# Optimization experiments

Hardware: AMD Instinct MI355X
Metric: run time of the kernel (lower is better)

Reference implementation:

```python
import jax, jax.numpy as jnp
import numpy as np

TOP_K = 2


def setup_inputs() -> dict:
    key = jax.random.key(0)
    k1, k2, k3, k4 = jax.random.split(key, 4)
    B, S, D, F, E = 4, 512, 512, 2048, 16
    hidden_states = jax.random.normal(k1, (B, S, D), dtype=jnp.float32)
    gate_weight = jax.random.normal(k2, (E, D), dtype=jnp.float32) * 0.02
    w1 = jax.random.normal(k3, (E, F, D), dtype=jnp.float32) * 0.02
    w2 = jax.random.normal(k4, (E, D, F), dtype=jnp.float32) * 0.02
    return {"hidden_states": hidden_states, "gate_weight": gate_weight, "w1": w1, "w2": w2}


def reference(hidden_states, gate_weight, w1, w2):
    B, S, D = hidden_states.shape
    E = gate_weight.shape[0]
    x = hidden_states.reshape(-1, D)  # [T, D]

    # fused_top_k_routing: logits = x @ Wg^T, top-k, softmax over the k values
    gate_logits = x @ gate_weight.T  # [T, E]
    top_vals, top_idx = jax.lax.top_k(gate_logits, TOP_K)  # [T, k]
    routing_w = jax.nn.softmax(top_vals, axis=-1)  # [T, k]

    # _prepare_expert_inputs: token t goes to expert e iff e in its top-k
    mask = jnp.any(top_idx[:, :, None] == jnp.arange(E)[None, None, :], axis=1)  # [T, E] bool

    # Expert FFN on routed tokens, computed densely over (token, expert) pairs then masked.
    # h[t,e,f] = silu(x_t @ W1_e^T)
    h = jax.nn.silu(jnp.einsum('td,efd->tef', x, w1))  # [T, E, F]
    counts = jnp.sum(mask, axis=0)  # [E]
    h_sum = jnp.einsum('tef,te->ef', h, mask.astype(h.dtype))  # [E, F]
    h_mean = h_sum / jnp.maximum(counts, 1)[:, None].astype(h.dtype)

    # fused_expert_scatter_gather uses expert_outputs[e].mean(dim=0);
    # mean(W2 @ act) = W2 @ mean(act) since W2 is linear.
    y_mean = jnp.einsum('ef,edf->ed', h_mean, w2)  # [E, D]
    y_mean = jnp.where((counts > 0)[:, None], y_mean, 0.0)

    # per-token combine: sum_k w_k * mean_output[expert_k]
    out = jnp.einsum('tk,tkd->td', routing_w, y_mean[top_idx])  # [T, D]
    return out.reshape(B, S, D)
```

## Files before the change

kernel.cpp:

```cpp
#include <hip/hip_runtime.h>

#define NTOK   2048
#define DIM    512
#define FDIM   2048
#define NEXP   16
#define CAP    768
#define BT2    128
#define NTB    (CAP / BT2)

typedef __bf16 bf16x8 __attribute__((ext_vector_type(8)));
typedef __bf16 bf16x4 __attribute__((ext_vector_type(4)));
typedef float  floatx4 __attribute__((ext_vector_type(4)));

#define WS_COUNTS    0
#define WS_ZEROPAGE  1024
#define WS_TOPIDX    4096
#define WS_ROUTW     20480
#define WS_HMEAN     36864
#define WS_YMEAN     167936
#define WS_XG        200704
#define WS_ZERO_BYTES 167936

__global__ __launch_bounds__(256) void k1_route_gather(
    const float* __restrict__ x, const float* __restrict__ gw,
    int* __restrict__ counts, int* __restrict__ top_idx,
    float* __restrict__ routw, __bf16* __restrict__ Xg)
{
    __shared__ float xt[16 * DIM];
    __shared__ float lg[16][17];
    __shared__ int   gdst[16][2];
    const int tid = threadIdx.x;
    const int t0  = blockIdx.x * 16;

    {
        const float4* src = (const float4*)(x + (size_t)t0 * DIM);
        float4* dst = (float4*)xt;
        #pragma unroll
        for (int i = 0; i < 8; ++i) dst[i * 256 + tid] = src[i * 256 + tid];
    }
    __syncthreads();

    {
        const int tl = tid >> 4, e = tid & 15;
        const float4* xr = (const float4*)(xt + tl * DIM);
        const float4* gr = (const float4*)(gw + e * DIM);
        float acc = 0.f;
        #pragma unroll 8
        for (int j = 0; j < DIM / 4; ++j) {
            float4 a = xr[j], b = gr[j];
            acc += a.x * b.x + a.y * b.y + a.z * b.z + a.w * b.w;
        }
        lg[tl][e] = acc;
    }
    __syncthreads();

    if (tid < 16) {
        const int tl = tid;
        float v0 = -1e30f, v1 = -1e30f; int i0 = 0, i1 = 0;
        #pragma unroll
        for (int e = 0; e < NEXP; ++e) {
            float v = lg[tl][e];
            if (v > v0)      { v1 = v0; i1 = i0; v0 = v; i0 = e; }
            else if (v > v1) { v1 = v;  i1 = e; }
        }
        float e1 = __expf(v1 - v0);
        float w0 = 1.f / (1.f + e1);
        float w1 = 1.f - w0;
        const int t = t0 + tl;
        top_idx[t * 2]     = i0; top_idx[t * 2 + 1] = i1;
        routw[t * 2]       = w0; routw[t * 2 + 1]   = w1;
        int p0 = atomicAdd(counts + i0, 1);
        int p1 = atomicAdd(counts + i1, 1);
        gdst[tl][0] = (p0 < CAP) ? (i0 * CAP + p0) : -1;
        gdst[tl][1] = (p1 < CAP) ? (i1 * CAP + p1) : -1;
    }
    __syncthreads();

    #pragma unroll
    for (int it = 0; it < 16; ++it) {
        int s   = it * 256 + tid;
        int job = s >> 7, el = s & 127;
        int tl  = job >> 1, k = job & 1;
        int dst = gdst[tl][k];
        if (dst >= 0) {
            float4 v = ((const float4*)(xt + tl * DIM))[el];
            bf16x4 o = { (__bf16)v.x, (__bf16)v.y, (__bf16)v.z, (__bf16)v.w };
            *(bf16x4*)(Xg + (size_t)dst * DIM + el * 4) = o;
        }
    }
}

__global__ __launch_bounds__(256) void k2_expert_ffn(
    const float* __restrict__ w1, const __bf16* __restrict__ Xg,
    const int* __restrict__ counts, const __bf16* __restrict__ zp,
    float* __restrict__ hmean)
{
    __shared__ __align__(16) __bf16 w1s[8 * 65 * 8];
    __shared__ __align__(16) __bf16 xs[8 * 129 * 8];
    __shared__ float hred[64][2];

    const int tid = threadIdx.x;
    const int bid = blockIdx.x;
    const int tb  = bid >> 9;
    const int rem = bid & 511;
    const int e   = rem & 15;
    const int f0  = (rem >> 4) * 64;
    const int cnt = min(counts[e], CAP);
    if (tb * BT2 >= cnt) return;
    const float inv = 1.f / (float)cnt;

    const int wv   = tid >> 6;
    const int lane = tid & 63;
    const int q    = lane >> 4;
    const int l15  = lane & 15;
    const int fsub = (wv & 1) * 32;
    const int tsub = (wv >> 1) * 64;

    floatx4 acc[2][4];
    #pragma unroll
    for (int a = 0; a < 2; ++a)
        #pragma unroll
        for (int b = 0; b < 4; ++b) acc[a][b] = (floatx4)0.f;

    for (int c = 0; c < 8; ++c) {
        const int d0 = c * 64;
        __syncthreads();
        #pragma unroll
        for (int it = 0; it < 2; ++it) {
            int s = it * 256 + tid;
            int f = s >> 3, g = s & 7;
            const float* src = w1 + ((size_t)(e * FDIM + f0 + f)) * DIM + d0 + g * 8;
            float4 a = ((const float4*)src)[0];
            float4 b = ((const float4*)src)[1];
            bf16x8 v;
            v[0] = (__bf16)a.x; v[1] = (__bf16)a.y; v[2] = (__bf16)a.z; v[3] = (__bf16)a.w;
            v[4] = (__bf16)b.x; v[5] = (__bf16)b.y; v[6] = (__bf16)b.z; v[7] = (__bf16)b.w;
            *(bf16x8*)(w1s + ((size_t)g * 65 + f) * 8) = v;
        }
        {
            const int kg = tid & 7;
            const int r0 = tid >> 3;
            #pragma unroll
            for (int it = 0; it < 4; ++it) {
                int t = it * 32 + r0;
                int r = tb * BT2 + t;
                const __bf16* src = (r < cnt)
                    ? (Xg + ((size_t)(e * CAP + r)) * DIM + d0 + kg * 8)
                    : zp;
                uint4 d = *(const uint4*)src;
                *(uint4*)(xs + ((size_t)kg * 129 + t) * 8) = d;
            }
        }
        __syncthreads();
        #pragma unroll
        for (int ks = 0; ks < 2; ++ks) {
            const int kg = ks * 4 + q;
            bf16x8 af0 = *(const bf16x8*)(w1s + (kg * 65 + fsub + l15) * 8);
            bf16x8 af1 = *(const bf16x8*)(w1s + (kg * 65 + fsub + 16 + l15) * 8);
            #pragma unroll
            for (int tt = 0; tt < 4; ++tt) {
                bf16x8 bfr = *(const bf16x8*)(xs + (kg * 129 + tsub + tt * 16 + l15) * 8);
                acc[0][tt] = __builtin_amdgcn_mfma_f32_16x16x32_bf16(af0, bfr, acc[0][tt], 0, 0, 0);
                acc[1][tt] = __builtin_amdgcn_mfma_f32_16x16x32_bf16(af1, bfr, acc[1][tt], 0, 0, 0);
            }
        }
    }

    float hs[8];
    #pragma unroll
    for (int i = 0; i < 8; ++i) hs[i] = 0.f;
    #pragma unroll
    for (int fa = 0; fa < 2; ++fa)
        #pragma unroll
        for (int tt = 0; tt < 4; ++tt)
            #pragma unroll
            for (int r = 0; r < 4; ++r) {
                float v = acc[fa][tt][r];
                hs[fa * 4 + r] += v / (1.f + __expf(-v));
            }

    #pragma unroll
    for (int i = 0; i < 8; ++i) {
        float v = hs[i];
        v += __shfl_xor(v, 1);
        v += __shfl_xor(v, 2);
        v += __shfl_xor(v, 4);
        v += __shfl_xor(v, 8);
        hs[i] = v;
    }
    if (l15 == 0) {
        #pragma unroll
        for (int fa = 0; fa < 2; ++fa)
            #pragma unroll
            for (int r = 0; r < 4; ++r) {
                int row = fsub + fa * 16 + q * 4 + r;
                hred[row][wv >> 1] = hs[fa * 4 + r];
            }
    }
    __syncthreads();
    if (tid < 64)
        atomicAdd(hmean + (size_t)e * FDIM + f0 + tid,
                  (hred[tid][0] + hred[tid][1]) * inv);
}

__global__ __launch_bounds__(256) void k3_ymean(
    const float* __restrict__ w2, const float* __restrict__ hmean,
    const int* __restrict__ counts, float* __restrict__ ymean)
{
    __shared__ float hl[FDIM];
    const int tid = threadIdx.x;
    const int bid = blockIdx.x;
    const int e   = bid >> 7;
    const int d0  = (bid & 127) * 4;

    {
        const float4* hg = (const float4*)(hmean + (size_t)e * FDIM);
        float4* hl4 = (float4*)hl;
        hl4[tid]       = hg[tid];
        hl4[256 + tid] = hg[256 + tid];
    }
    __syncthreads();

    const int wv = tid >> 6, lane = tid & 63;
    const int d = d0 + wv;
    const float4* wr  = (const float4*)(w2 + ((size_t)e * DIM + d) * FDIM);
    const float4* hl4 = (const float4*)hl;
    float acc = 0.f;
    #pragma unroll
    for (int i = 0; i < 8; ++i) {
        float4 a = wr[i * 64 + lane];
        float4 h = hl4[i * 64 + lane];
        acc += a.x * h.x + a.y * h.y + a.z * h.z + a.w * h.w;
    }
    #pragma unroll
    for (int m = 1; m < 64; m <<= 1) acc += __shfl_xor(acc, m);
    if (lane == 0)
        ymean[e * DIM + d] = (counts[e] > 0) ? acc : 0.f;
}

__global__ __launch_bounds__(256) void k4_combine(
    const int* __restrict__ top_idx, const float* __restrict__ routw,
    const float* __restrict__ ymean, float* __restrict__ out)
{
    const int idx = blockIdx.x * 256 + threadIdx.x;
    const int t = idx >> 7;
    const int c = idx & 127;
    const int i0 = top_idx[t * 2], i1 = top_idx[t * 2 + 1];
    const float w0 = routw[t * 2], w1 = routw[t * 2 + 1];
    float4 a = ((const float4*)(ymean + (size_t)i0 * DIM))[c];
    float4 b = ((const float4*)(ymean + (size_t)i1 * DIM))[c];
    float4 o;
    o.x = w0 * a.x + w1 * b.x;
    o.y = w0 * a.y + w1 * b.y;
    o.z = w0 * a.z + w1 * b.z;
    o.w = w0 * a.w + w1 * b.w;
    ((float4*)out)[idx] = o;
}

extern "C" void kernel_launch(void* const* d_in, const int* in_sizes, int n_in,
                              void* d_out, int out_size, void* d_ws, size_t ws_size,
                              hipStream_t stream)
{
    (void)in_sizes; (void)n_in; (void)out_size; (void)ws_size;
    const float* x  = (const float*)d_in[0];
    const float* gw = (const float*)d_in[1];
    const float* w1 = (const float*)d_in[2];
    const float* w2 = (const float*)d_in[3];
    float* out = (float*)d_out;

    char* ws = (char*)d_ws;
    int*    counts  = (int*)   (ws + WS_COUNTS);
    const __bf16* zp = (const __bf16*)(ws + WS_ZEROPAGE);
    int*    top_idx = (int*)   (ws + WS_TOPIDX);
    float*  routw   = (float*) (ws + WS_ROUTW);
    float*  hmean   = (float*) (ws + WS_HMEAN);
    float*  ymean   = (float*) (ws + WS_YMEAN);
    __bf16* Xg      = (__bf16*)(ws + WS_XG);

    hipMemsetAsync(d_ws, 0, WS_ZERO_BYTES, stream);

    k1_route_gather<<<dim3(NTOK / 16), dim3(256), 0, stream>>>(x, gw, counts, top_idx, routw, Xg);
    k2_expert_ffn  <<<dim3(NTB * 32 * NEXP), dim3(256), 0, stream>>>(w1, Xg, counts, zp, hmean);
    k3_ymean       <<<dim3(NEXP * 128), dim3(256), 0, stream>>>(w2, hmean, counts, ymean);
    k4_combine     <<<dim3(NTOK * DIM / 4 / 256), dim3(256), 0, stream>>>(top_idx, routw, ymean, out);
}
```

Measured before the change: 212.9 us.

## Restructure expert FFN: resident W1 slice, loop token chunks with async double-buffered loads

Each block now owns a 32-wide F slice of one expert and keeps the full W1 slice (all of D) in shared memory, converted to bf16 once. It then loops over every token chunk for that expert, staging activations with async global-to-LDS loads into a double buffer. Before, W1 was reloaded for every token tile. Because one block now covers all tokens for its slice, the atomicAdd becomes a plain store and the memset shrinks to just the counts region. The cost is fewer blocks (1024) whose work grows with the expert's token count, which risks load imbalance across experts and lower occupancy from the larger LDS footprint.

```diff
diff --git a/kernel.cpp b/kernel.cpp
--- a/kernel.cpp
+++ b/kernel.cpp
@@ -5,8 +5,8 @@
 #define FDIM   2048
 #define NEXP   16
 #define CAP    768
-#define BT2    128
-#define NTB    (CAP / BT2)
+#define FT     32
+#define TC     128
 
 typedef __bf16 bf16x8 __attribute__((ext_vector_type(8)));
 typedef __bf16 bf16x4 __attribute__((ext_vector_type(4)));
@@ -19,7 +19,13 @@
 #define WS_HMEAN     36864
 #define WS_YMEAN     167936
 #define WS_XG        200704
-#define WS_ZERO_BYTES 167936
+#define WS_ZERO_BYTES 2048
+
+__device__ __forceinline__ void async_lds16(const void* g, void* l) {
+    __builtin_amdgcn_global_load_lds(
+        (__attribute__((address_space(1))) void*)(void*)g,
+        (__attribute__((address_space(3))) void*)l, 16, 0, 0);
+}
 
 __global__ __launch_bounds__(256) void k1_route_gather(
     const float* __restrict__ x, const float* __restrict__ gw,
@@ -95,112 +101,118 @@
     const int* __restrict__ counts, const __bf16* __restrict__ zp,
     float* __restrict__ hmean)
 {
-    __shared__ __align__(16) __bf16 w1s[8 * 65 * 8];
-    __shared__ __align__(16) __bf16 xs[8 * 129 * 8];
-    __shared__ float hred[64][2];
+    __shared__ __align__(16) __bf16 w1s[64 * 33 * 8];
+    __shared__ __align__(16) __bf16 xs[2][8 * 128 * 8];
+    __shared__ float hred[FT][4];
 
     const int tid = threadIdx.x;
     const int bid = blockIdx.x;
-    const int tb  = bid >> 9;
-    const int rem = bid & 511;
-    const int e   = rem & 15;
-    const int f0  = (rem >> 4) * 64;
+    const int e   = ((bid & 7) << 1) | (bid >> 9);
+    const int f0  = ((bid >> 3) & 63) * FT;
     const int cnt = min(counts[e], CAP);
-    if (tb * BT2 >= cnt) return;
-    const float inv = 1.f / (float)cnt;
+    const float inv = 1.f / (float)max(cnt, 1);
 
     const int wv   = tid >> 6;
     const int lane = tid & 63;
     const int q    = lane >> 4;
     const int l15  = lane & 15;
-    const int fsub = (wv & 1) * 32;
-    const int tsub = (wv >> 1) * 64;
-
-    floatx4 acc[2][4];
+    const int tsub = wv * 32;
+
+    const int nchunk = (cnt + TC - 1) / TC;
+    const int total  = nchunk * 8;
+
+    auto STAGE = [&](int b, int tc, int c) {
+        __bf16* dst0 = xs[b];
+        #pragma unroll
+        for (int it = 0; it < 4; ++it) {
+            int base = it * 256 + wv * 64;
+            int slot = base + lane;
+            int kg = slot >> 7, t = slot & 127;
+            int r  = tc * TC + t;
+            const __bf16* src = (r < cnt)
+                ? (Xg + ((size_t)(e * CAP + r)) * DIM + c * 64 + kg * 8)
+                : zp;
+            async_lds16(src, dst0 + (size_t)base * 8);
+        }
+    };
+
+    if (total > 0) STAGE(0, 0, 0);
+
+    #pragma unroll
+    for (int it = 0; it < 8; ++it) {
+        int s = it * 256 + tid;
+        int kg = s & 63, f = s >> 6;
+        const float* src = w1 + ((size_t)(e * FDIM + f0 + f)) * DIM + kg * 8;
+        float4 a = ((const float4*)src)[0];
+        float4 b = ((const float4*)src)[1];
+        bf16x8 v;
+        v[0] = (__bf16)a.x; v[1] = (__bf16)a.y; v[2] = (__bf16)a.z; v[3] = (__bf16)a.w;
+        v[4] = (__bf16)b.x; v[5] = (__bf16)b.y; v[6] = (__bf16)b.z; v[7] = (__bf16)b.w;
+        *(bf16x8*)(w1s + ((size_t)kg * 33 + f) * 8) = v;
+    }
+    __syncthreads();
+
+    floatx4 acc[2][2];
     #pragma unroll
     for (int a = 0; a < 2; ++a)
         #pragma unroll
-        for (int b = 0; b < 4; ++b) acc[a][b] = (floatx4)0.f;
-
-    for (int c = 0; c < 8; ++c) {
-        const int d0 = c * 64;
+        for (int b = 0; b < 2; ++b) acc[a][b] = (floatx4)0.f;
+    float rs[2][4] = {{0.f, 0.f, 0.f, 0.f}, {0.f, 0.f, 0.f, 0.f}};
+
+    for (int g = 0; g < total; ++g) {
+        const int cur = g & 1;
+        const int c   = g & 7;
+        if (g + 1 < total) STAGE(cur ^ 1, (g + 1) >> 3, (g + 1) & 7);
+
+        const __bf16* xb = xs[cur];
+        #pragma unroll
+        for (int ks = 0; ks < 2; ++ks) {
+            int kga = c * 8 + ks * 4 + q;
+            int kl  = ks * 4 + q;
+            bf16x8 a0 = *(const bf16x8*)(w1s + ((size_t)kga * 33 + l15) * 8);
+            bf16x8 a1 = *(const bf16x8*)(w1s + ((size_t)kga * 33 + 16 + l15) * 8);
+            bf16x8 b0 = *(const bf16x8*)(xb + ((size_t)kl * 128 + tsub + l15) * 8);
+            bf16x8 b1 = *(const bf16x8*)(xb + ((size_t)kl * 128 + tsub + 16 + l15) * 8);
+            acc[0][0] = __builtin_amdgcn_mfma_f32_16x16x32_bf16(a0, b0, acc[0][0], 0, 0, 0);
+            acc[0][1] = __builtin_amdgcn_mfma_f32_16x16x32_bf16(a0, b1, acc[0][1], 0, 0, 0);
+            acc[1][0] = __builtin_amdgcn_mfma_f32_16x16x32_bf16(a1, b0, acc[1][0], 0, 0, 0);
+            acc[1][1] = __builtin_amdgcn_mfma_f32_16x16x32_bf16(a1, b1, acc[1][1], 0, 0, 0);
+        }
+        if (c == 7) {
+            #pragma unroll
+            for (int fa = 0; fa < 2; ++fa)
+                #pragma unroll
+                for (int r = 0; r < 4; ++r) {
+                    float v0 = acc[fa][0][r], v1 = acc[fa][1][r];
+                    rs[fa][r] += v0 / (1.f + __expf(-v0)) + v1 / (1.f + __expf(-v1));
+                    acc[fa][0][r] = 0.f; acc[fa][1][r] = 0.f;
+                }
+        }
         __syncthreads();
-        #pragma unroll
-        for (int it = 0; it < 2; ++it) {
-            int s = it * 256 + tid;
-            int f = s >> 3, g = s & 7;
-            const float* src = w1 + ((size_t)(e * FDIM + f0 + f)) * DIM + d0 + g * 8;
-            float4 a = ((const float4*)src)[0];
-            float4 b = ((const float4*)src)[1];
-            bf16x8 v;
-            v[0] = (__bf16)a.x; v[1] = (__bf16)a.y; v[2] = (__bf16)a.z; v[3] = (__bf16)a.w;
-            v[4] = (__bf16)b.x; v[5] = (__bf16)b.y; v[6] = (__bf16)b.z; v[7] = (__bf16)b.w;
-            *(bf16x8*)(w1s + ((size_t)g * 65 + f) * 8) = v;
-        }
-        {
-            const int kg = tid & 7;
-            const int r0 = tid >> 3;
-            #pragma unroll
-            for (int it = 0; it < 4; ++it) {
-                int t = it * 32 + r0;
-                int r = tb * BT2 + t;
-                const __bf16* src = (r < cnt)
-                    ? (Xg + ((size_t)(e * CAP + r)) * DIM + d0 + kg * 8)
-                    : zp;
-                uint4 d = *(const uint4*)src;
-                *(uint4*)(xs + ((size_t)kg * 129 + t) * 8) = d;
-            }
-        }
-        __syncthreads();
-        #pragma unroll
-        for (int ks = 0; ks < 2; ++ks) {
-            const int kg = ks * 4 + q;
-            bf16x8 af0 = *(const bf16x8*)(w1s + (kg * 65 + fsub + l15) * 8);
-            bf16x8 af1 = *(const bf16x8*)(w1s + (kg * 65 + fsub + 16 + l15) * 8);
-            #pragma unroll
-            for (int tt = 0; tt < 4; ++tt) {
-                bf16x8 bfr = *(const bf16x8*)(xs + (kg * 129 + tsub + tt * 16 + l15) * 8);
-                acc[0][tt] = __builtin_amdgcn_mfma_f32_16x16x32_bf16(af0, bfr, acc[0][tt], 0, 0, 0);
-                acc[1][tt] = __builtin_amdgcn_mfma_f32_16x16x32_bf16(af1, bfr, acc[1][tt], 0, 0, 0);
-            }
-        }
-    }
-
-    float hs[8];
-    #pragma unroll
-    for (int i = 0; i < 8; ++i) hs[i] = 0.f;
+    }
+
     #pragma unroll
     for (int fa = 0; fa < 2; ++fa)
         #pragma unroll
-        for (int tt = 0; tt < 4; ++tt)
-            #pragma unroll
-            for (int r = 0; r < 4; ++r) {
-                float v = acc[fa][tt][r];
-                hs[fa * 4 + r] += v / (1.f + __expf(-v));
-            }
-
-    #pragma unroll
-    for (int i = 0; i < 8; ++i) {
-        float v = hs[i];
-        v += __shfl_xor(v, 1);
-        v += __shfl_xor(v, 2);
-        v += __shfl_xor(v, 4);
-        v += __shfl_xor(v, 8);
-        hs[i] = v;
-    }
+        for (int r = 0; r < 4; ++r) {
+            float v = rs[fa][r];
+            v += __shfl_xor(v, 1);
+            v += __shfl_xor(v, 2);
+            v += __shfl_xor(v, 4);
+            v += __shfl_xor(v, 8);
+            rs[fa][r] = v;
+        }
     if (l15 == 0) {
         #pragma unroll
         for (int fa = 0; fa < 2; ++fa)
             #pragma unroll
-            for (int r = 0; r < 4; ++r) {
-                int row = fsub + fa * 16 + q * 4 + r;
-                hred[row][wv >> 1] = hs[fa * 4 + r];
-            }
-    }
-    __syncthreads();
-    if (tid < 64)
-        atomicAdd(hmean + (size_t)e * FDIM + f0 + tid,
-                  (hred[tid][0] + hred[tid][1]) * inv);
+            for (int r = 0; r < 4; ++r)
+                hred[fa * 16 + q * 4 + r][wv] = rs[fa][r];
+    }
+    __syncthreads();
+    if (tid < FT)
+        hmean[(size_t)e * FDIM + f0 + tid] =
+            (hred[tid][0] + hred[tid][1] + hred[tid][2] + hred[tid][3]) * inv;
 }
 
 __global__ __launch_bounds__(256) void k3_ymean(
@@ -280,7 +292,7 @@
     hipMemsetAsync(d_ws, 0, WS_ZERO_BYTES, stream);
 
     k1_route_gather<<<dim3(NTOK / 16), dim3(256), 0, stream>>>(x, gw, counts, top_idx, routw, Xg);
-    k2_expert_ffn  <<<dim3(NTB * 32 * NEXP), dim3(256), 0, stream>>>(w1, Xg, counts, zp, hmean);
+    k2_expert_ffn  <<<dim3(NEXP * (FDIM / FT)), dim3(256), 0, stream>>>(w1, Xg, counts, zp, hmean);
     k3_ymean       <<<dim3(NEXP * 128), dim3(256), 0, stream>>>(w2, hmean, counts, ymean);
     k4_combine     <<<dim3(NTOK * DIM / 4 / 256), dim3(256), 0, stream>>>(top_idx, routw, ymean, out);
 }
```

Result: slower. 234.3 us (+10.1%).

## Double-buffer expert FFN LDS tiles with async global-to-LDS loads

Applied to the files above, without the earlier changes.

Adds double buffering to the k2 expert FFN mainloop. The next chunk's w1 values are prefetched into registers and the next Xg chunk is staged straight into LDS with global_load_lds while the MFMAs run on the current buffer. The goal is to overlap global memory latency with compute and to drop one barrier per iteration. It doubles the LDS footprint, removes the padding on the xs rows (possible bank conflicts), and needs the async LDS loads to have finished before the single barrier.

```diff
diff --git a/kernel.cpp b/kernel.cpp
--- a/kernel.cpp
+++ b/kernel.cpp
@@ -20,6 +20,12 @@
 #define WS_YMEAN     167936
 #define WS_XG        200704
 #define WS_ZERO_BYTES 167936
+
+__device__ __forceinline__ void async_lds16(const void* g, void* l) {
+    __builtin_amdgcn_global_load_lds(
+        (__attribute__((address_space(1))) void*)(void*)g,
+        (__attribute__((address_space(3))) void*)l, 16, 0, 0);
+}
 
 __global__ __launch_bounds__(256) void k1_route_gather(
     const float* __restrict__ x, const float* __restrict__ gw,
@@ -95,8 +101,8 @@
     const int* __restrict__ counts, const __bf16* __restrict__ zp,
     float* __restrict__ hmean)
 {
-    __shared__ __align__(16) __bf16 w1s[8 * 65 * 8];
-    __shared__ __align__(16) __bf16 xs[8 * 129 * 8];
+    __shared__ __align__(16) __bf16 w1s[2][8 * 65 * 8];
+    __shared__ __align__(16) __bf16 xs[2][8 * 128 * 8];
     __shared__ float hred[64][2];
 
     const int tid = threadIdx.x;
@@ -116,53 +122,78 @@
     const int fsub = (wv & 1) * 32;
     const int tsub = (wv >> 1) * 64;
 
+    const int wfA = tid >> 3,        wgA = tid & 7;
+    const int wfB = (256 + tid) >> 3, wgB = (256 + tid) & 7;
+    const float* w1rowA = w1 + ((size_t)(e * FDIM + f0 + wfA)) * DIM + wgA * 8;
+    const float* w1rowB = w1 + ((size_t)(e * FDIM + f0 + wfB)) * DIM + wgB * 8;
+
+    float4 wa0, wb0, wa1, wb1;
+
+    auto ISSUE_W1 = [&](int c) {
+        const float* pA = w1rowA + c * 64;
+        const float* pB = w1rowB + c * 64;
+        wa0 = ((const float4*)pA)[0]; wb0 = ((const float4*)pA)[1];
+        wa1 = ((const float4*)pB)[0]; wb1 = ((const float4*)pB)[1];
+    };
+    auto WRITE_W1 = [&](int b) {
+        bf16x8 v;
+        v[0] = (__bf16)wa0.x; v[1] = (__bf16)wa0.y; v[2] = (__bf16)wa0.z; v[3] = (__bf16)wa0.w;
+        v[4] = (__bf16)wb0.x; v[5] = (__bf16)wb0.y; v[6] = (__bf16)wb0.z; v[7] = (__bf16)wb0.w;
+        *(bf16x8*)(&w1s[b][0] + ((size_t)wgA * 65 + wfA) * 8) = v;
+        v[0] = (__bf16)wa1.x; v[1] = (__bf16)wa1.y; v[2] = (__bf16)wa1.z; v[3] = (__bf16)wa1.w;
+        v[4] = (__bf16)wb1.x; v[5] = (__bf16)wb1.y; v[6] = (__bf16)wb1.z; v[7] = (__bf16)wb1.w;
+        *(bf16x8*)(&w1s[b][0] + ((size_t)wgB * 65 + wfB) * 8) = v;
+    };
+    auto STAGE_X = [&](int b, int c) {
+        __bf16* dst0 = &xs[b][0];
+        #pragma unroll
+        for (int it = 0; it < 4; ++it) {
+            int base = it * 256 + wv * 64;
+            int slot = base + lane;
+            int kg = slot >> 7, t = slot & 127;
+            int r  = tb * BT2 + t;
+            const __bf16* src = (r < cnt)
+                ? (Xg + ((size_t)(e * CAP + r)) * DIM + c * 64 + kg * 8)
+                : zp;
+            async_lds16(src, dst0 + (size_t)base * 8);
+        }
+    };
+
+    ISSUE_W1(0);
+    STAGE_X(0, 0);
+    WRITE_W1(0);
+    __syncthreads();
+
     floatx4 acc[2][4];
     #pragma unroll
     for (int a = 0; a < 2; ++a)
         #pragma unroll
         for (int b = 0; b < 4; ++b) acc[a][b] = (floatx4)0.f;
 
+    int cur = 0;
     for (int c = 0; c < 8; ++c) {
-        const int d0 = c * 64;
-        __syncthreads();
-        #pragma unroll
-        for (int it = 0; it < 2; ++it) {
-            int s = it * 256 + tid;
-            int f = s >> 3, g = s & 7;
-            const float* src = w1 + ((size_t)(e * FDIM + f0 + f)) * DIM + d0 + g * 8;
-            float4 a = ((const float4*)src)[0];
-            float4 b = ((const float4*)src)[1];
-            bf16x8 v;
-            v[0] = (__bf16)a.x; v[1] = (__bf16)a.y; v[2] = (__bf16)a.z; v[3] = (__bf16)a.w;
-            v[4] = (__bf16)b.x; v[5] = (__bf16)b.y; v[6] = (__bf16)b.z; v[7] = (__bf16)b.w;
-            *(bf16x8*)(w1s + ((size_t)g * 65 + f) * 8) = v;
-        }
-        {
-            const int kg = tid & 7;
-            const int r0 = tid >> 3;
-            #pragma unroll
-            for (int it = 0; it < 4; ++it) {
-                int t = it * 32 + r0;
-                int r = tb * BT2 + t;
-                const __bf16* src = (r < cnt)
-                    ? (Xg + ((size_t)(e * CAP + r)) * DIM + d0 + kg * 8)
-                    : zp;
-                uint4 d = *(const uint4*)src;
-                *(uint4*)(xs + ((size_t)kg * 129 + t) * 8) = d;
-            }
-        }
-        __syncthreads();
+        if (c < 7) {
+            ISSUE_W1(c + 1);
+            STAGE_X(cur ^ 1, c + 1);
+        }
+        const __bf16* wp = &w1s[cur][0];
+        const __bf16* xp = &xs[cur][0];
         #pragma unroll
         for (int ks = 0; ks < 2; ++ks) {
             const int kg = ks * 4 + q;
-            bf16x8 af0 = *(const bf16x8*)(w1s + (kg * 65 + fsub + l15) * 8);
-            bf16x8 af1 = *(const bf16x8*)(w1s + (kg * 65 + fsub + 16 + l15) * 8);
+            bf16x8 a0 = *(const bf16x8*)(wp + ((size_t)kg * 65 + fsub + l15) * 8);
+            bf16x8 a1 = *(const bf16x8*)(wp + ((size_t)kg * 65 + fsub + 16 + l15) * 8);
             #pragma unroll
             for (int tt = 0; tt < 4; ++tt) {
-                bf16x8 bfr = *(const bf16x8*)(xs + (kg * 129 + tsub + tt * 16 + l15) * 8);
-                acc[0][tt] = __builtin_amdgcn_mfma_f32_16x16x32_bf16(af0, bfr, acc[0][tt], 0, 0, 0);
-                acc[1][tt] = __builtin_amdgcn_mfma_f32_16x16x32_bf16(af1, bfr, acc[1][tt], 0, 0, 0);
+                bf16x8 bfr = *(const bf16x8*)(xp + ((size_t)kg * 128 + tsub + tt * 16 + l15) * 8);
+                acc[0][tt] = __builtin_amdgcn_mfma_f32_16x16x32_bf16(a0, bfr, acc[0][tt], 0, 0, 0);
+                acc[1][tt] = __builtin_amdgcn_mfma_f32_16x16x32_bf16(a1, bfr, acc[1][tt], 0, 0, 0);
             }
+        }
+        if (c < 7) {
+            WRITE_W1(cur ^ 1);
+            __syncthreads();
+            cur ^= 1;
         }
     }
 
```

Result: slower. 218.4 us (+2.6%).

## Register-prefetch next K-chunk in expert FFN and zero hmean in routing kernel

Applied to the files above, without the earlier changes.

The expert FFN main loop now issues the global loads for the next 64-wide K chunk of W1 and gathered tokens into registers before the MFMA work on the current chunk. The loaded values are written to shared memory at the start of the next iteration, so global latency overlaps compute and only one barrier is needed per iteration. Separately, the hmean buffer is zeroed inside the routing kernel, which shrinks the workspace memset to the counts and zero-page region. The prefetch raises register pressure and adds a hand-written waitcnt and barrier sequence.

```diff
diff --git a/kernel.cpp b/kernel.cpp
--- a/kernel.cpp
+++ b/kernel.cpp
@@ -19,18 +19,21 @@
 #define WS_HMEAN     36864
 #define WS_YMEAN     167936
 #define WS_XG        200704
-#define WS_ZERO_BYTES 167936
+#define WS_ZERO_BYTES 2048
 
 __global__ __launch_bounds__(256) void k1_route_gather(
     const float* __restrict__ x, const float* __restrict__ gw,
     int* __restrict__ counts, int* __restrict__ top_idx,
-    float* __restrict__ routw, __bf16* __restrict__ Xg)
+    float* __restrict__ routw, __bf16* __restrict__ Xg,
+    float* __restrict__ hmean)
 {
     __shared__ float xt[16 * DIM];
     __shared__ float lg[16][17];
     __shared__ int   gdst[16][2];
     const int tid = threadIdx.x;
     const int t0  = blockIdx.x * 16;
+
+    hmean[blockIdx.x * 256 + tid] = 0.f;
 
     {
         const float4* src = (const float4*)(x + (size_t)t0 * DIM);
@@ -116,6 +119,48 @@
     const int fsub = (wv & 1) * 32;
     const int tsub = (wv >> 1) * 64;
 
+    const int wfA = tid >> 3, wgA = tid & 7;
+    const int wfB = wfA + 32;
+    const float* w1pA = w1 + ((size_t)(e * FDIM + f0 + wfA)) * DIM + wgA * 8;
+    const float* w1pB = w1 + ((size_t)(e * FDIM + f0 + wfB)) * DIM + wgA * 8;
+    const int xkg = tid & 7, xr0 = tid >> 3;
+
+    float4 wa0, wb0, wa1, wb1;
+    uint4  xv0, xv1, xv2, xv3;
+
+    auto ISSUE = [&](int c) {
+        const int d0 = c * 64;
+        wa0 = ((const float4*)(w1pA + d0))[0];
+        wb0 = ((const float4*)(w1pA + d0))[1];
+        wa1 = ((const float4*)(w1pB + d0))[0];
+        wb1 = ((const float4*)(w1pB + d0))[1];
+        const __bf16* xb = Xg + (size_t)e * CAP * DIM + d0 + xkg * 8;
+        int r0 = tb * BT2 + xr0;
+        const __bf16* s0 = (r0       < cnt) ? (xb + (size_t)(r0      ) * DIM) : zp;
+        const __bf16* s1 = (r0 +  32 < cnt) ? (xb + (size_t)(r0 +  32) * DIM) : zp;
+        const __bf16* s2 = (r0 +  64 < cnt) ? (xb + (size_t)(r0 +  64) * DIM) : zp;
+        const __bf16* s3 = (r0 +  96 < cnt) ? (xb + (size_t)(r0 +  96) * DIM) : zp;
+        xv0 = *(const uint4*)s0;
+        xv1 = *(const uint4*)s1;
+        xv2 = *(const uint4*)s2;
+        xv3 = *(const uint4*)s3;
+    };
+    auto WRITE = [&]() {
+        bf16x8 v;
+        v[0] = (__bf16)wa0.x; v[1] = (__bf16)wa0.y; v[2] = (__bf16)wa0.z; v[3] = (__bf16)wa0.w;
+        v[4] = (__bf16)wb0.x; v[5] = (__bf16)wb0.y; v[6] = (__bf16)wb0.z; v[7] = (__bf16)wb0.w;
+        *(bf16x8*)(w1s + ((size_t)wgA * 65 + wfA) * 8) = v;
+        v[0] = (__bf16)wa1.x; v[1] = (__bf16)wa1.y; v[2] = (__bf16)wa1.z; v[3] = (__bf16)wa1.w;
+        v[4] = (__bf16)wb1.x; v[5] = (__bf16)wb1.y; v[6] = (__bf16)wb1.z; v[7] = (__bf16)wb1.w;
+        *(bf16x8*)(w1s + ((size_t)wgA * 65 + wfB) * 8) = v;
+        *(uint4*)(xs + ((size_t)xkg * 129 + xr0      ) * 8) = xv0;
+        *(uint4*)(xs + ((size_t)xkg * 129 + xr0 +  32) * 8) = xv1;
+        *(uint4*)(xs + ((size_t)xkg * 129 + xr0 +  64) * 8) = xv2;
+        *(uint4*)(xs + ((size_t)xkg * 129 + xr0 +  96) * 8) = xv3;
+    };
+
+    ISSUE(0);
+
     floatx4 acc[2][4];
     #pragma unroll
     for (int a = 0; a < 2; ++a)
@@ -123,35 +168,13 @@
         for (int b = 0; b < 4; ++b) acc[a][b] = (floatx4)0.f;
 
     for (int c = 0; c < 8; ++c) {
-        const int d0 = c * 64;
         __syncthreads();
-        #pragma unroll
-        for (int it = 0; it < 2; ++it) {
-            int s = it * 256 + tid;
-            int f = s >> 3, g = s & 7;
-            const float* src = w1 + ((size_t)(e * FDIM + f0 + f)) * DIM + d0 + g * 8;
-            float4 a = ((const float4*)src)[0];
-            float4 b = ((const float4*)src)[1];
-            bf16x8 v;
-            v[0] = (__bf16)a.x; v[1] = (__bf16)a.y; v[2] = (__bf16)a.z; v[3] = (__bf16)a.w;
-            v[4] = (__bf16)b.x; v[5] = (__bf16)b.y; v[6] = (__bf16)b.z; v[7] = (__bf16)b.w;
-            *(bf16x8*)(w1s + ((size_t)g * 65 + f) * 8) = v;
-        }
-        {
-            const int kg = tid & 7;
-            const int r0 = tid >> 3;
-            #pragma unroll
-            for (int it = 0; it < 4; ++it) {
-                int t = it * 32 + r0;
-                int r = tb * BT2 + t;
-                const __bf16* src = (r < cnt)
-                    ? (Xg + ((size_t)(e * CAP + r)) * DIM + d0 + kg * 8)
-                    : zp;
-                uint4 d = *(const uint4*)src;
-                *(uint4*)(xs + ((size_t)kg * 129 + t) * 8) = d;
-            }
-        }
-        __syncthreads();
+        WRITE();
+        if (c < 7) ISSUE(c + 1);
+        asm volatile("s_waitcnt lgkmcnt(0)" ::: "memory");
+        __builtin_amdgcn_sched_barrier(0);
+        __builtin_amdgcn_s_barrier();
+        __builtin_amdgcn_sched_barrier(0);
         #pragma unroll
         for (int ks = 0; ks < 2; ++ks) {
             const int kg = ks * 4 + q;
@@ -279,7 +302,7 @@
 
     hipMemsetAsync(d_ws, 0, WS_ZERO_BYTES, stream);
 
-    k1_route_gather<<<dim3(NTOK / 16), dim3(256), 0, stream>>>(x, gw, counts, top_idx, routw, Xg);
+    k1_route_gather<<<dim3(NTOK / 16), dim3(256), 0, stream>>>(x, gw, counts, top_idx, routw, Xg, hmean);
     k2_expert_ffn  <<<dim3(NTB * 32 * NEXP), dim3(256), 0, stream>>>(w1, Xg, counts, zp, hmean);
     k3_ymean       <<<dim3(NEXP * 128), dim3(256), 0, stream>>>(w2, hmean, counts, ymean);
     k4_combine     <<<dim3(NTOK * DIM / 4 / 256), dim3(256), 0, stream>>>(top_idx, routw, ymean, out);
```

Result: no change. 212.3 us (-0.3%).
